# Kernel tuning notes

Hardware: AMD Instinct MI355X
Metric: run time of the kernel (lower is better)

## Reference

```python
import jax, jax.numpy as jnp
import numpy as np

B, T, V, D = 128, 512, 8000, 256
H = D // 2   # per-direction LSTM hidden
L = 4        # label_dim


def setup_inputs() -> dict:
    key = jax.random.key(0)
    ks = jax.random.split(key, 16)
    s = 0.1
    pad_seq = jax.random.randint(ks[0], (B, T), 0, V)
    lens = jax.random.randint(ks[1], (B,), 1, T + 1)
    lens = lens.at[0].set(T)  # padded length == max(lens), as pad_packed_sequence would give
    emb = (jax.random.normal(ks[2], (V, D)) * s).at[0].set(0.0)  # padding_idx=0
    return {
        "pad_seq": pad_seq, "lens": lens, "emb": emb,
        "W_ih_f": jax.random.normal(ks[3], (4 * H, D)) * s,
        "W_hh_f": jax.random.normal(ks[4], (4 * H, H)) * s,
        "b_ih_f": jax.random.normal(ks[5], (4 * H,)) * s,
        "b_hh_f": jax.random.normal(ks[6], (4 * H,)) * s,
        "W_ih_b": jax.random.normal(ks[7], (4 * H, D)) * s,
        "W_hh_b": jax.random.normal(ks[8], (4 * H, H)) * s,
        "b_ih_b": jax.random.normal(ks[9], (4 * H,)) * s,
        "b_hh_b": jax.random.normal(ks[10], (4 * H,)) * s,
        "W_lab": jax.random.normal(ks[11], (L, D)) * s,
        "b_lab": jax.random.normal(ks[12], (L,)) * s,
        "transitions": jax.random.normal(ks[13], (L, L)),
        "from_BOS": jax.random.normal(ks[14], (L,)),
        "to_EOS": jax.random.normal(ks[15], (L,)),
    }


def _lstm(xs_t, mask_t, Wih, Whh, bih, bhh, reverse):
    """Masked unidirectional LSTM over time-major xs_t [T,B,D]; emulates
    pack_padded_sequence semantics (state frozen and output zeroed at pads)."""
    nb, nh = xs_t.shape[1], Whh.shape[1]

    def step(carry, inp):
        h, c = carry
        x_t, m_t = inp  # [B,D], [B,1] bool
        g = x_t @ Wih.T + bih + h @ Whh.T + bhh
        i, f, gg, o = jnp.split(g, 4, axis=-1)
        c2 = jax.nn.sigmoid(f) * c + jax.nn.sigmoid(i) * jnp.tanh(gg)
        h2 = jax.nn.sigmoid(o) * jnp.tanh(c2)
        h = jnp.where(m_t, h2, h)
        c = jnp.where(m_t, c2, c)
        return (h, c), jnp.where(m_t, h2, 0.0)

    init = (jnp.zeros((nb, nh), xs_t.dtype), jnp.zeros((nb, nh), xs_t.dtype))
    _, ys = jax.lax.scan(step, init, (xs_t, mask_t), reverse=reverse)
    return ys  # [T,B,H]


def reference(pad_seq, lens, emb, W_ih_f, W_hh_f, b_ih_f, b_hh_f,
              W_ih_b, W_hh_b, b_ih_b, b_hh_b, W_lab, b_lab,
              transitions, from_BOS, to_EOS):
    b, t = pad_seq.shape
    x = emb[pad_seq]                       # [B,T,D]
    xs_t = jnp.transpose(x, (1, 0, 2))     # [T,B,D]
    mask_t = (jnp.arange(t)[:, None] < lens[None, :])[:, :, None]  # [T,B,1]

    hf = _lstm(xs_t, mask_t, W_ih_f, W_hh_f, b_ih_f, b_hh_f, reverse=False)
    hb = _lstm(xs_t, mask_t, W_ih_b, W_hh_b, b_ih_b, b_hh_b, reverse=True)
    h = jnp.concatenate([hf, hb], axis=-1)           # [T,B,D]
    scores = h @ W_lab.T + b_lab                     # [T,B,L] emissions

    # --- Viterbi forward pass ---
    best0 = from_BOS[None, :] + scores[0]            # [B,L]

    def vstep(best, inp):
        ti, e = inp                                  # step index, emissions [B,L]
        smat = best[:, :, None] + e[:, None, :] + transitions[None]  # [B,prev,cur]
        valid = (lens > ti)[:, None]
        nb = jnp.where(valid, smat.max(axis=1), best)
        return nb, jnp.argmax(smat, axis=1)          # backtrace [B,L]

    bestT, bt = jax.lax.scan(vstep, best0, (jnp.arange(1, t), scores[1:]))
    final_vec = bestT + to_EOS[None, :]              # [B,L]
    last_lab = jnp.argmax(final_vec, axis=1)         # [B]

    # --- backtrace: label[t] = bt[t][label[t+1]] for t < len-1 ---
    bt_pad = jnp.concatenate([bt, jnp.zeros((1,) + bt.shape[1:], bt.dtype)], axis=0)  # [T,B,L]

    def bstep(cur, inp):
        ti, bt_t = inp
        cand = jnp.take_along_axis(bt_t, cur[:, None], axis=1)[:, 0]
        cur = jnp.where(ti == lens - 1, last_lab,
                        jnp.where(ti < lens - 1, cand, cur))
        return cur, cur

    _, labs = jax.lax.scan(bstep, jnp.zeros((b,), last_lab.dtype),
                           (jnp.arange(t), bt_pad), reverse=True)
    labels = labs.T  # [B,T]
    len_bool = jnp.arange(t)[None, :] < lens[:, None]
    return labels * len_bool
```

## Files before the change

kernel.cpp:

```cpp
#include <hip/hip_runtime.h>
#include <math.h>

#define VOCAB 8000
#define BATCH 128
#define TMAX  512
#define DIM   256
#define HID   128
#define G4    512
#define NCOL  1024

__device__ __forceinline__ float dpp_xor1(float x) {
  int r = __builtin_amdgcn_update_dpp(0, __builtin_bit_cast(int, x),
                                      0xB1, 0xF, 0xF, true);
  return __builtin_bit_cast(float, r);
}
__device__ __forceinline__ float dpp_xor2(float x) {
  int r = __builtin_amdgcn_update_dpp(0, __builtin_bit_cast(int, x),
                                      0x4E, 0xF, 0xF, true);
  return __builtin_bit_cast(float, r);
}
__device__ __forceinline__ unsigned dpp_xor1u(unsigned x) {
  return (unsigned)__builtin_amdgcn_update_dpp(0, (int)x, 0xB1, 0xF, 0xF, true);
}
__device__ __forceinline__ unsigned dpp_xor2u(unsigned x) {
  return (unsigned)__builtin_amdgcn_update_dpp(0, (int)x, 0x4E, 0xF, 0xF, true);
}
__device__ __forceinline__ float dpp_bc0(float x) {
  int r = __builtin_amdgcn_update_dpp(0, __builtin_bit_cast(int, x),
                                      0x00, 0xF, 0xF, true);
  return __builtin_bit_cast(float, r);
}
__device__ __forceinline__ float dpp_bc1(float x) {
  int r = __builtin_amdgcn_update_dpp(0, __builtin_bit_cast(int, x),
                                      0x55, 0xF, 0xF, true);
  return __builtin_bit_cast(float, r);
}
__device__ __forceinline__ float dpp_bc2(float x) {
  int r = __builtin_amdgcn_update_dpp(0, __builtin_bit_cast(int, x),
                                      0xAA, 0xF, 0xF, true);
  return __builtin_bit_cast(float, r);
}
__device__ __forceinline__ float dpp_bc3(float x) {
  int r = __builtin_amdgcn_update_dpp(0, __builtin_bit_cast(int, x),
                                      0xFF, 0xF, 0xF, true);
  return __builtin_bit_cast(float, r);
}

__device__ __forceinline__ void bar_lds() {
  asm volatile("s_waitcnt lgkmcnt(0)" ::: "memory");
  __builtin_amdgcn_s_barrier();
}

__global__ __launch_bounds__(256) void embw_gemm(
    const float* __restrict__ emb,
    const float* __restrict__ Wf, const float* __restrict__ Wb,
    const float* __restrict__ bihf, const float* __restrict__ bhhf,
    const float* __restrict__ bihb, const float* __restrict__ bhhb,
    float* __restrict__ embW) {
  __shared__ float As[32][132];
  __shared__ float Bs[32][132];
  const int tid = threadIdx.x;
  const int m0 = blockIdx.x * 128;
  const int n0 = blockIdx.y * 128;
  const int tx = tid & 15, ty = tid >> 4;
  const int lrow = tid >> 1;
  const int lseg = (tid & 1) * 16;
  const float* Wsrc = (n0 < 512) ? Wf : Wb;
  const int nbase = (n0 < 512) ? n0 : (n0 - 512);

  float acc[8][8];
  #pragma unroll
  for (int i = 0; i < 8; ++i)
    #pragma unroll
    for (int jj = 0; jj < 8; ++jj) acc[i][jj] = 0.f;

  for (int k0 = 0; k0 < 256; k0 += 32) {
    const int gm = m0 + lrow;
    #pragma unroll
    for (int q = 0; q < 4; ++q) {
      float4 v = make_float4(0.f, 0.f, 0.f, 0.f);
      if (gm < VOCAB) v = *(const float4*)(emb + (size_t)gm * 256 + k0 + lseg + 4 * q);
      As[lseg + 4*q + 0][lrow] = v.x;
      As[lseg + 4*q + 1][lrow] = v.y;
      As[lseg + 4*q + 2][lrow] = v.z;
      As[lseg + 4*q + 3][lrow] = v.w;
    }
    #pragma unroll
    for (int q = 0; q < 4; ++q) {
      float4 v = *(const float4*)(Wsrc + (size_t)(nbase + lrow) * 256 + k0 + lseg + 4 * q);
      Bs[lseg + 4*q + 0][lrow] = v.x;
      Bs[lseg + 4*q + 1][lrow] = v.y;
      Bs[lseg + 4*q + 2][lrow] = v.z;
      Bs[lseg + 4*q + 3][lrow] = v.w;
    }
    __syncthreads();
    #pragma unroll
    for (int k = 0; k < 32; ++k) {
      float4 av0 = *(const float4*)&As[k][ty * 8];
      float4 av1 = *(const float4*)&As[k][ty * 8 + 4];
      float4 bv0 = *(const float4*)&Bs[k][tx * 4];
      float4 bv1 = *(const float4*)&Bs[k][64 + tx * 4];
      float a[8]  = {av0.x, av0.y, av0.z, av0.w, av1.x, av1.y, av1.z, av1.w};
      float bb[8] = {bv0.x, bv0.y, bv0.z, bv0.w, bv1.x, bv1.y, bv1.z, bv1.w};
      #pragma unroll
      for (int i = 0; i < 8; ++i)
        #pragma unroll
        for (int jj = 0; jj < 8; ++jj)
          acc[i][jj] += a[i] * bb[jj];
    }
    __syncthreads();
  }

  float bias[8];
  #pragma unroll
  for (int jj = 0; jj < 8; ++jj) {
    int n = n0 + ((jj < 4) ? (tx * 4 + jj) : (64 + tx * 4 + (jj - 4)));
    bias[jj] = (n < 512) ? (bihf[n] + bhhf[n]) : (bihb[n - 512] + bhhb[n - 512]);
  }
  #pragma unroll
  for (int i = 0; i < 8; ++i) {
    int gm = m0 + ty * 8 + i;
    if (gm >= VOCAB) continue;
    float4 v0 = make_float4(acc[i][0] + bias[0], acc[i][1] + bias[1],
                            acc[i][2] + bias[2], acc[i][3] + bias[3]);
    float4 v1 = make_float4(acc[i][4] + bias[4], acc[i][5] + bias[5],
                            acc[i][6] + bias[6], acc[i][7] + bias[7]);
    *(float4*)(embW + (size_t)gm * NCOL + n0 + tx * 4) = v0;
    *(float4*)(embW + (size_t)gm * NCOL + n0 + 64 + tx * 4) = v1;
  }
}

#define REP8(M) M(0) M(1) M(2) M(3) M(4) M(5) M(6) M(7)
#define REP8G(M,G) M(G,0) M(G,1) M(G,2) M(G,3) M(G,4) M(G,5) M(G,6) M(G,7)

__global__ __launch_bounds__(512)
__attribute__((amdgpu_waves_per_eu(2, 2)))
void lstm_rec(
    const int* __restrict__ pad_seq, const int* __restrict__ lens,
    const float* __restrict__ Whh_f, const float* __restrict__ Whh_b,
    const float* __restrict__ embW, const float* __restrict__ W_lab,
    float* __restrict__ e_part) {
  const int dir = blockIdx.x & 1;
  const int b   = blockIdx.x >> 1;
  const int tid = threadIdx.x;
  const int j   = tid >> 2;
  const int q   = tid & 3;
  const int parity = q & 1;
  const int half   = (q >> 1) & 1;

  __shared__ float ring[8][4][36];
  __shared__ float wls[4][132];
  __shared__ int   tok[TMAX];

  tok[tid] = pad_seq[b * TMAX + tid];
  wls[tid >> 7][tid & 127] = W_lab[(tid >> 7) * DIM + dir * HID + (tid & 127)];
  if (tid < 144) ((float*)ring)[tid] = 0.f;

  const int len = lens[b];
  const float* __restrict__ Whh = dir ? Whh_b : Whh_f;

  const float4* wr0 = (const float4*)(Whh + (size_t)(0 * HID + j) * HID + 32 * q);
  const float4* wr1 = (const float4*)(Whh + (size_t)(1 * HID + j) * HID + 32 * q);
  const float4* wr2 = (const float4*)(Whh + (size_t)(2 * HID + j) * HID + 32 * q);
  const float4* wr3 = (const float4*)(Whh + (size_t)(3 * HID + j) * HID + 32 * q);
#define DECLW(G,I)                                                      \
  float w##G##_##I##_0, w##G##_##I##_1, w##G##_##I##_2, w##G##_##I##_3; \
  { float4 t = wr##G[I];                                                \
    w##G##_##I##_0 = t.x; w##G##_##I##_1 = t.y;                         \
    w##G##_##I##_2 = t.z; w##G##_##I##_3 = t.w; }                       \
  asm volatile("" : "+v"(w##G##_##I##_0));                              \
  asm volatile("" : "+v"(w##G##_##I##_1));                              \
  asm volatile("" : "+v"(w##G##_##I##_2));                              \
  asm volatile("" : "+v"(w##G##_##I##_3));
  REP8G(DECLW,0) REP8G(DECLW,1) REP8G(DECLW,2) REP8G(DECLW,3)
#undef DECLW

#define KEEPW(G,I)                                                      \
  asm volatile("" : "+v"(w##G##_##I##_0), "+v"(w##G##_##I##_1),         \
                    "+v"(w##G##_##I##_2), "+v"(w##G##_##I##_3));

  float c = 0.f;
  const float ascale = (q == 2) ? 2.f : 1.f;
  const float* __restrict__ ecol = embW + dir * G4 + (q * HID + j);
  float* __restrict__ ep = e_part + (size_t)(dir * BATCH + b) * TMAX * 4;

  bar_lds();

  float xb0, xb1, xb2, xb3, xb4, xb5, xb6, xb7;
#define PRE(r) { const int ss = nbase + r; xb##r = 0.f;                 \
    if (ss < len) {                                                     \
      const int tt = dir ? (len - 1 - ss) : ss;                         \
      xb##r = ecol[(size_t)tok[tt] * NCOL]; } }
  { const int nbase = 0; REP8(PRE) }

#define MACC(G,I)                                         \
    a##G##0 = fmaf(hv##I.x, w##G##_##I##_0, a##G##0);     \
    a##G##1 = fmaf(hv##I.y, w##G##_##I##_1, a##G##1);     \
    a##G##2 = fmaf(hv##I.z, w##G##_##I##_2, a##G##2);     \
    a##G##3 = fmaf(hv##I.w, w##G##_##I##_3, a##G##3);

#define STEP(r, XW)                                                     \
  {                                                                     \
    const float4* h4 = (const float4*)&ring[r][q][0];                   \
    float4 hv0 = h4[0], hv1 = h4[1], hv2 = h4[2], hv3 = h4[3];          \
    float4 hv4 = h4[4], hv5 = h4[5], hv6 = h4[6], hv7 = h4[7];          \
    float a00=0.f,a01=0.f,a02=0.f,a03=0.f;                              \
    float a10=0.f,a11=0.f,a12=0.f,a13=0.f;                              \
    float a20=0.f,a21=0.f,a22=0.f,a23=0.f;                              \
    float a30=0.f,a31=0.f,a32=0.f,a33=0.f;                              \
    REP8G(MACC,0) REP8G(MACC,1) REP8G(MACC,2) REP8G(MACC,3)             \
    const float p0 = (a00+a01)+(a02+a03);                               \
    const float p1 = (a10+a11)+(a12+a13);                               \
    const float p2 = (a20+a21)+(a22+a23);                               \
    const float p3 = (a30+a31)+(a32+a33);                               \
     \
    const float klo = parity ? p1 : p0, slo = parity ? p0 : p1;         \
    const float khi = parity ? p3 : p2, shi = parity ? p2 : p3;         \
    const float alo = klo + dpp_xor1(slo);                              \
    const float ahi = khi + dpp_xor1(shi);                              \
    const float kb = half ? ahi : alo, sb = half ? alo : ahi;           \
    const float tot = kb + dpp_xor2(sb);                                \
    const float aa = tot + (XW);                                        \
    const float sg = 1.f / (1.f + __expf(-ascale * aa));                \
    const float act = (q == 2) ? (2.f * sg - 1.f) : sg;                 \
                          \
    const float e1 = dpp_xor1(act);                                     \
    const float e2 = dpp_xor2(act);                                     \
    const float e3 = dpp_xor2(e1);                                      \
    const float ev  = parity ? e1 : act, od  = parity ? act : e1;       \
    const float ev2 = parity ? e3 : e2,  od2 = parity ? e2 : e3;        \
    const float ig = half ? ev2 : ev, fg = half ? od2 : od;             \
    const float gt = half ? ev : ev2, og = half ? od : od2;             \
    c = fg * c + ig * gt;                                               \
    const float s2 = 1.f / (1.f + __expf(-2.f * c));                    \
    const float hh = og * (2.f * s2 - 1.f);                             \
    if (q == 0) ring[(r + 1) & 7][j >> 5][j & 31] = hh;                 \
    bar_lds();                                                          \
  }

  for (int s0 = 0; s0 < len; s0 += 8) {
    REP8G(KEEPW,0) REP8G(KEEPW,1) REP8G(KEEPW,2) REP8G(KEEPW,3)
    const int cnt = (len - s0 < 8) ? (len - s0) : 8;
    STEP(0, xb0)
    if (cnt > 1) STEP(1, xb1)
    if (cnt > 2) STEP(2, xb2)
    if (cnt > 3) STEP(3, xb3)
    if (cnt > 4) STEP(4, xb4)
    if (cnt > 5) STEP(5, xb5)
    if (cnt > 6) STEP(6, xb6)
    if (cnt > 7) STEP(7, xb7)
    { const int nbase = s0 + 8; REP8(PRE) }
    {
      const int r = tid >> 6, l = (tid >> 4) & 3, sub = tid & 15;
      if (r < cnt) {
        const float4* hp = (const float4*)&ring[(r + 1) & 7][sub >> 2][8 * (sub & 3)];
        const float4 h0 = hp[0], h1 = hp[1];
        const float4* wp = (const float4*)&wls[l][8 * sub];
        const float4 u0 = wp[0], u1 = wp[1];
        float d = h0.x*u0.x + h0.y*u0.y + h0.z*u0.z + h0.w*u0.w
                + h1.x*u1.x + h1.y*u1.y + h1.z*u1.z + h1.w*u1.w;
        d += dpp_xor1(d); d += dpp_xor2(d);
        d += __shfl_xor(d, 4); d += __shfl_xor(d, 8);
        if (sub == 0) {
          const int ss = s0 + r;
          const int tt = dir ? (len - 1 - ss) : ss;
          ep[tt * 4 + l] = d;
        }
      }
    }
    bar_lds();
  }
#undef STEP
#undef MACC
#undef PRE
#undef KEEPW
}

__global__ __launch_bounds__(512) void viterbi_k(
    const int* __restrict__ lens, const float* __restrict__ e_part,
    const float* __restrict__ b_lab, const float* __restrict__ trans,
    const float* __restrict__ from_BOS, const float* __restrict__ to_EOS,
    int* __restrict__ out) {
  const int b = blockIdx.x;
  const int tid = threadIdx.x;
  __shared__ float sc[TMAX][4];
  __shared__ unsigned btm[TMAX];
  __shared__ int labs[TMAX];
  const int len = lens[b];

  if (tid < len) {
    const float4 f  = *(const float4*)(e_part + ((size_t)b * TMAX + tid) * 4);
    const float4 g2 = *(const float4*)(e_part + ((size_t)(BATCH + b) * TMAX + tid) * 4);
    const float4 bl = *(const float4*)b_lab;
    sc[tid][0] = f.x + g2.x + bl.x;
    sc[tid][1] = f.y + g2.y + bl.y;
    sc[tid][2] = f.z + g2.z + bl.z;
    sc[tid][3] = f.w + g2.w + bl.w;
  }
  __syncthreads();

  if (tid < 4) {
    const int l = tid;
    float trc0 = trans[0 * 4 + l], trc1 = trans[1 * 4 + l];
    float trc2 = trans[2 * 4 + l], trc3 = trans[3 * 4 + l];
    float best = from_BOS[l] + sc[0][l];
    float e_next = sc[1][l];
    for (int ti = 1; ti < len; ++ti) {
      const float e = e_next;
      e_next = sc[(ti + 1 < TMAX) ? ti + 1 : ti][l];
      const float b0 = dpp_bc0(best);
      const float b1 = dpp_bc1(best);
      const float b2 = dpp_bc2(best);
      const float b3 = dpp_bc3(best);
      float m = (b0 + e) + trc0; int arg = 0;
      float v;
      v = (b1 + e) + trc1; if (v > m) { m = v; arg = 1; }
      v = (b2 + e) + trc2; if (v > m) { m = v; arg = 2; }
      v = (b3 + e) + trc3; if (v > m) { m = v; arg = 3; }
      best = m;
      unsigned av = ((unsigned)arg) << (8 * l);
      av |= dpp_xor1u(av);
      av |= dpp_xor2u(av);
      if (l == 0) btm[ti] = av;
    }
    const float f0 = dpp_bc0(best) + to_EOS[0];
    const float f1 = dpp_bc1(best) + to_EOS[1];
    const float f2 = dpp_bc2(best) + to_EOS[2];
    const float f3 = dpp_bc3(best) + to_EOS[3];
    if (l == 0) {
      float m = f0; int last = 0;
      if (f1 > m) { m = f1; last = 1; }
      if (f2 > m) { m = f2; last = 2; }
      if (f3 > m) { m = f3; last = 3; }
      labs[len - 1] = last;
      int cur = last;
      #pragma unroll 4
      for (int ti = len - 2; ti >= 0; --ti) {
        cur = (int)((btm[ti + 1] >> (8 * cur)) & 255u);
        labs[ti] = cur;
      }
    }
  }
  __syncthreads();
  out[b * TMAX + tid] = (tid < len) ? labs[tid] : 0;
}

extern "C" void kernel_launch(void* const* d_in, const int* in_sizes, int n_in,
                              void* d_out, int out_size, void* d_ws, size_t ws_size,
                              hipStream_t stream) {
  const int*   pad_seq  = (const int*)d_in[0];
  const int*   lens     = (const int*)d_in[1];
  const float* emb      = (const float*)d_in[2];
  const float* W_ih_f   = (const float*)d_in[3];
  const float* W_hh_f   = (const float*)d_in[4];
  const float* b_ih_f   = (const float*)d_in[5];
  const float* b_hh_f   = (const float*)d_in[6];
  const float* W_ih_b   = (const float*)d_in[7];
  const float* W_hh_b   = (const float*)d_in[8];
  const float* b_ih_b   = (const float*)d_in[9];
  const float* b_hh_b   = (const float*)d_in[10];
  const float* W_lab    = (const float*)d_in[11];
  const float* b_lab    = (const float*)d_in[12];
  const float* trans    = (const float*)d_in[13];
  const float* from_BOS = (const float*)d_in[14];
  const float* to_EOS   = (const float*)d_in[15];
  int* out = (int*)d_out;

  float* embW   = (float*)d_ws;
  float* e_part = embW + (size_t)VOCAB * NCOL;

  embw_gemm<<<dim3(63, 8), 256, 0, stream>>>(emb, W_ih_f, W_ih_b,
                                             b_ih_f, b_hh_f, b_ih_b, b_hh_b, embW);
  lstm_rec<<<dim3(2 * BATCH), 512, 0, stream>>>(pad_seq, lens, W_hh_f, W_hh_b,
                                                embW, W_lab, e_part);
  viterbi_k<<<dim3(BATCH), 512, 0, stream>>>(lens, e_part, b_lab, trans,
                                             from_BOS, to_EOS, out);
}
```

Before: 577.3 us.

## Double-buffer embedding GEMM tiles and enlarge M tile to 256 rows

The vocabulary-by-gate-weights GEMM now uses a 256x128 block tile with a 16x8 register tile per thread. It double-buffers LDS, prefetching the next K slice into registers while computing the current one, which cuts the barriers per K step to one. The grid shrinks from 63x8 to 32x8 blocks. This gives more arithmetic per byte loaded and hides global load latency, at the cost of higher register pressure (128 accumulators plus prefetch registers) and fewer blocks to spread across the CUs.

Measured after the change: 1.048 ms. 1.82x slower.

```diff
diff --git a/kernel.cpp b/kernel.cpp
--- a/kernel.cpp
+++ b/kernel.cpp
@@ -51,75 +51,116 @@
   __builtin_amdgcn_s_barrier();
 }
 
-__global__ __launch_bounds__(256) void embw_gemm(
+__global__ __launch_bounds__(256, 1) void embw_gemm(
     const float* __restrict__ emb,
     const float* __restrict__ Wf, const float* __restrict__ Wb,
     const float* __restrict__ bihf, const float* __restrict__ bhhf,
     const float* __restrict__ bihb, const float* __restrict__ bhhb,
     float* __restrict__ embW) {
-  __shared__ float As[32][132];
-  __shared__ float Bs[32][132];
+  __shared__ float As[2][32][260];
+  __shared__ float Bs[2][32][132];
   const int tid = threadIdx.x;
-  const int m0 = blockIdx.x * 128;
+  const int m0 = blockIdx.x * 256;
   const int n0 = blockIdx.y * 128;
   const int tx = tid & 15, ty = tid >> 4;
   const int lrow = tid >> 1;
   const int lseg = (tid & 1) * 16;
   const float* Wsrc = (n0 < 512) ? Wf : Wb;
   const int nbase = (n0 < 512) ? n0 : (n0 - 512);
-
-  float acc[8][8];
+  const int gmA = m0 + tid;
+
+  float acc[16][8];
   #pragma unroll
-  for (int i = 0; i < 8; ++i)
+  for (int i = 0; i < 16; ++i)
     #pragma unroll
-    for (int jj = 0; jj < 8; ++jj) acc[i][jj] = 0.f;
-
-  for (int k0 = 0; k0 < 256; k0 += 32) {
-    const int gm = m0 + lrow;
-    #pragma unroll
-    for (int q = 0; q < 4; ++q) {
-      float4 v = make_float4(0.f, 0.f, 0.f, 0.f);
-      if (gm < VOCAB) v = *(const float4*)(emb + (size_t)gm * 256 + k0 + lseg + 4 * q);
-      As[lseg + 4*q + 0][lrow] = v.x;
-      As[lseg + 4*q + 1][lrow] = v.y;
-      As[lseg + 4*q + 2][lrow] = v.z;
-      As[lseg + 4*q + 3][lrow] = v.w;
-    }
-    #pragma unroll
-    for (int q = 0; q < 4; ++q) {
-      float4 v = *(const float4*)(Wsrc + (size_t)(nbase + lrow) * 256 + k0 + lseg + 4 * q);
-      Bs[lseg + 4*q + 0][lrow] = v.x;
-      Bs[lseg + 4*q + 1][lrow] = v.y;
-      Bs[lseg + 4*q + 2][lrow] = v.z;
-      Bs[lseg + 4*q + 3][lrow] = v.w;
-    }
-    __syncthreads();
+    for (int j = 0; j < 8; ++j) acc[i][j] = 0.f;
+
+  float4 ra0, ra1, ra2, ra3, ra4, ra5, ra6, ra7;
+  float4 rb0, rb1, rb2, rb3;
+
+#define LOADT(K0)                                                       \
+  {                                                                     \
+    ra0 = ra1 = ra2 = ra3 = make_float4(0.f, 0.f, 0.f, 0.f);            \
+    ra4 = ra5 = ra6 = ra7 = make_float4(0.f, 0.f, 0.f, 0.f);            \
+    if (gmA < VOCAB) {                                                  \
+      const float* ap = emb + (size_t)gmA * 256 + (K0);                 \
+      ra0 = *(const float4*)(ap + 0);  ra1 = *(const float4*)(ap + 4);  \
+      ra2 = *(const float4*)(ap + 8);  ra3 = *(const float4*)(ap + 12); \
+      ra4 = *(const float4*)(ap + 16); ra5 = *(const float4*)(ap + 20); \
+      ra6 = *(const float4*)(ap + 24); ra7 = *(const float4*)(ap + 28); \
+    }                                                                   \
+    const float* bp = Wsrc + (size_t)(nbase + lrow) * 256 + (K0) + lseg;\
+    rb0 = *(const float4*)(bp + 0);  rb1 = *(const float4*)(bp + 4);    \
+    rb2 = *(const float4*)(bp + 8);  rb3 = *(const float4*)(bp + 12);   \
+  }
+
+#define WRITET(BUF)                                                     \
+  {                                                                     \
+    As[BUF][0][tid]  = ra0.x; As[BUF][1][tid]  = ra0.y;                 \
+    As[BUF][2][tid]  = ra0.z; As[BUF][3][tid]  = ra0.w;                 \
+    As[BUF][4][tid]  = ra1.x; As[BUF][5][tid]  = ra1.y;                 \
+    As[BUF][6][tid]  = ra1.z; As[BUF][7][tid]  = ra1.w;                 \
+    As[BUF][8][tid]  = ra2.x; As[BUF][9][tid]  = ra2.y;                 \
+    As[BUF][10][tid] = ra2.z; As[BUF][11][tid] = ra2.w;                 \
+    As[BUF][12][tid] = ra3.x; As[BUF][13][tid] = ra3.y;                 \
+    As[BUF][14][tid] = ra3.z; As[BUF][15][tid] = ra3.w;                 \
+    As[BUF][16][tid] = ra4.x; As[BUF][17][tid] = ra4.y;                 \
+    As[BUF][18][tid] = ra4.z; As[BUF][19][tid] = ra4.w;                 \
+    As[BUF][20][tid] = ra5.x; As[BUF][21][tid] = ra5.y;                 \
+    As[BUF][22][tid] = ra5.z; As[BUF][23][tid] = ra5.w;                 \
+    As[BUF][24][tid] = ra6.x; As[BUF][25][tid] = ra6.y;                 \
+    As[BUF][26][tid] = ra6.z; As[BUF][27][tid] = ra6.w;                 \
+    As[BUF][28][tid] = ra7.x; As[BUF][29][tid] = ra7.y;                 \
+    As[BUF][30][tid] = ra7.z; As[BUF][31][tid] = ra7.w;                 \
+    Bs[BUF][lseg + 0][lrow]  = rb0.x; Bs[BUF][lseg + 1][lrow]  = rb0.y; \
+    Bs[BUF][lseg + 2][lrow]  = rb0.z; Bs[BUF][lseg + 3][lrow]  = rb0.w; \
+    Bs[BUF][lseg + 4][lrow]  = rb1.x; Bs[BUF][lseg + 5][lrow]  = rb1.y; \
+    Bs[BUF][lseg + 6][lrow]  = rb1.z; Bs[BUF][lseg + 7][lrow]  = rb1.w; \
+    Bs[BUF][lseg + 8][lrow]  = rb2.x; Bs[BUF][lseg + 9][lrow]  = rb2.y; \
+    Bs[BUF][lseg + 10][lrow] = rb2.z; Bs[BUF][lseg + 11][lrow] = rb2.w; \
+    Bs[BUF][lseg + 12][lrow] = rb3.x; Bs[BUF][lseg + 13][lrow] = rb3.y; \
+    Bs[BUF][lseg + 14][lrow] = rb3.z; Bs[BUF][lseg + 15][lrow] = rb3.w; \
+  }
+
+  LOADT(0)
+  WRITET(0)
+  __syncthreads();
+
+  for (int kt = 0; kt < 8; ++kt) {
+    const int cur = kt & 1;
+    if (kt < 7) LOADT((kt + 1) * 32)
     #pragma unroll
     for (int k = 0; k < 32; ++k) {
-      float4 av0 = *(const float4*)&As[k][ty * 8];
-      float4 av1 = *(const float4*)&As[k][ty * 8 + 4];
-      float4 bv0 = *(const float4*)&Bs[k][tx * 4];
-      float4 bv1 = *(const float4*)&Bs[k][64 + tx * 4];
-      float a[8]  = {av0.x, av0.y, av0.z, av0.w, av1.x, av1.y, av1.z, av1.w};
+      float4 av0 = *(const float4*)&As[cur][k][ty * 16];
+      float4 av1 = *(const float4*)&As[cur][k][ty * 16 + 4];
+      float4 av2 = *(const float4*)&As[cur][k][ty * 16 + 8];
+      float4 av3 = *(const float4*)&As[cur][k][ty * 16 + 12];
+      float4 bv0 = *(const float4*)&Bs[cur][k][tx * 4];
+      float4 bv1 = *(const float4*)&Bs[cur][k][64 + tx * 4];
+      float a[16] = {av0.x, av0.y, av0.z, av0.w, av1.x, av1.y, av1.z, av1.w,
+                     av2.x, av2.y, av2.z, av2.w, av3.x, av3.y, av3.z, av3.w};
       float bb[8] = {bv0.x, bv0.y, bv0.z, bv0.w, bv1.x, bv1.y, bv1.z, bv1.w};
       #pragma unroll
-      for (int i = 0; i < 8; ++i)
+      for (int i = 0; i < 16; ++i)
         #pragma unroll
-        for (int jj = 0; jj < 8; ++jj)
-          acc[i][jj] += a[i] * bb[jj];
+        for (int j = 0; j < 8; ++j)
+          acc[i][j] += a[i] * bb[j];
     }
-    __syncthreads();
+    if (kt < 7) {
+      WRITET(cur ^ 1)
+      __syncthreads();
+    }
   }
 
   float bias[8];
   #pragma unroll
-  for (int jj = 0; jj < 8; ++jj) {
-    int n = n0 + ((jj < 4) ? (tx * 4 + jj) : (64 + tx * 4 + (jj - 4)));
-    bias[jj] = (n < 512) ? (bihf[n] + bhhf[n]) : (bihb[n - 512] + bhhb[n - 512]);
+  for (int j = 0; j < 8; ++j) {
+    int n = n0 + ((j < 4) ? (tx * 4 + j) : (64 + tx * 4 + (j - 4)));
+    bias[j] = (n < 512) ? (bihf[n] + bhhf[n]) : (bihb[n - 512] + bhhb[n - 512]);
   }
   #pragma unroll
-  for (int i = 0; i < 8; ++i) {
-    int gm = m0 + ty * 8 + i;
+  for (int i = 0; i < 16; ++i) {
+    int gm = m0 + ty * 16 + i;
     if (gm >= VOCAB) continue;
     float4 v0 = make_float4(acc[i][0] + bias[0], acc[i][1] + bias[1],
                             acc[i][2] + bias[2], acc[i][3] + bias[3]);
@@ -128,6 +169,8 @@
     *(float4*)(embW + (size_t)gm * NCOL + n0 + tx * 4) = v0;
     *(float4*)(embW + (size_t)gm * NCOL + n0 + 64 + tx * 4) = v1;
   }
+#undef LOADT
+#undef WRITET
 }
 
 #define REP8(M) M(0) M(1) M(2) M(3) M(4) M(5) M(6) M(7)
@@ -369,7 +412,7 @@
   float* embW   = (float*)d_ws;
   float* e_part = embW + (size_t)VOCAB * NCOL;
 
-  embw_gemm<<<dim3(63, 8), 256, 0, stream>>>(emb, W_ih_f, W_ih_b,
+  embw_gemm<<<dim3(32, 8), 256, 0, stream>>>(emb, W_ih_f, W_ih_b,
                                              b_ih_f, b_hh_f, b_ih_b, b_hh_b, embW);
   lstm_rec<<<dim3(2 * BATCH), 512, 0, stream>>>(pad_seq, lens, W_hh_f, W_hh_b,
                                                 embW, W_lab, e_part);
```
